# Kernel optimization log

Measured on AMD Instinct MI355X. Metric: run time of the kernel, lower is better.

## Reference

```python
import jax, jax.numpy as jnp
import numpy as np
import math

B = 32        # graphs in batch
N_PER = 2000  # nodes per graph
E_PER = 16000 # edges per graph
H = 256       # hidden_size
EF = 20       # edge_features
ET = 3        # edge_types
C = 100       # candidate nodes per graph
N = B * N_PER
E = B * E_PER


def setup_inputs() -> dict:
    key = jax.random.key(0)
    ks = jax.random.split(key, 12)
    embedding = jax.random.normal(ks[0], (N, H), dtype=jnp.float32)
    scores = jax.random.normal(ks[1], (N, 1), dtype=jnp.float32)
    offsets = jnp.arange(B, dtype=jnp.int64) * N_PER
    src = (jax.random.randint(ks[2], (B, E_PER), 0, N_PER) + offsets[:, None]).reshape(-1)
    dst = (jax.random.randint(ks[3], (B, E_PER), 0, N_PER) + offsets[:, None]).reshape(-1)
    etype = jax.random.randint(ks[4], (E,), 0, ET)
    cand_idx = offsets[:, None] + jnp.arange(C, dtype=jnp.int64)[None, :]  # [B, C]
    label = jax.random.randint(ks[5], (B,), 0, C)
    s = 1.0 / math.sqrt(H)
    Wl = jax.random.normal(ks[6], (H, H), dtype=jnp.float32) * s
    bl = jnp.zeros((H,), dtype=jnp.float32)
    Wr = jax.random.normal(ks[7], (H, H), dtype=jnp.float32) * s
    br = jnp.zeros((H,), dtype=jnp.float32)
    We = jax.random.normal(ks[8], (H, EF), dtype=jnp.float32) * (1.0 / math.sqrt(EF))
    be = jnp.zeros((H,), dtype=jnp.float32)
    edge_emb = jax.random.normal(ks[9], (ET, EF), dtype=jnp.float32)
    return {"embedding": embedding, "scores": scores, "Wl": Wl, "bl": bl,
            "Wr": Wr, "br": br, "We": We, "be": be, "edge_emb": edge_emb,
            "src": src, "dst": dst, "etype": etype, "cand_idx": cand_idx,
            "label": label}


def reference(embedding, scores, Wl, bl, Wr, br, We, be, edge_emb,
              src, dst, etype, cand_idx, label):
    # dropout is identity in eval mode
    h = embedding
    # edge type features: GELU(Embedding(type))  (torch GELU = exact erf form)
    ef = jax.nn.gelu(edge_emb[etype], approximate=False)          # [E, EF]
    attn_q = h @ Wl.T + bl                                         # [N, H]
    attn_k1 = h @ Wr.T + br                                        # [N, H]
    attn_k2 = ef @ We.T + be                                       # [E, H]
    # u_add_e: src node key + edge key
    attn_k = attn_k1[src] + attn_k2                                # [E, H]
    # v_dot_e: dst query dot edge key, scaled
    alpha = jnp.sum(attn_q[dst] * attn_k, axis=-1) / jnp.sqrt(jnp.float32(H))  # [E]
    # edge_softmax over incoming edges of each dst node
    seg_max = jax.ops.segment_max(alpha, dst, num_segments=N)
    ex = jnp.exp(alpha - seg_max[dst])
    seg_sum = jax.ops.segment_sum(ex, dst, num_segments=N)
    a = ex / seg_sum[dst]                                          # [E]
    # u_mul_e + sum aggregation: scatter-sum of src scores weighted by attention
    upd = jax.ops.segment_sum(scores[src] * a[:, None], dst, num_segments=N)  # [N, 1]
    # per-graph candidate logits and CE loss
    logits = upd[cand_idx.reshape(-1)].reshape(B, C)               # [B, C]
    logp = jax.nn.log_softmax(logits, axis=-1)
    loss = -jnp.sum(logp[jnp.arange(B), label])
    return loss, logits
```

## Files before the change

### kernel.cpp

```cpp
#include <hip/hip_runtime.h>
#include <hip/hip_bf16.h>
#include <float.h>
#include <math.h>

#define NB 32
#define NPER 2000
#define EPER 16000
#define HID 256
#define EFD 20
#define ETN 3
#define CN 100
#define NTOT (NB*NPER)
#define ETOT (NB*EPER)

#define QDELTA (6.0f/127.0f)
#define QINV   (127.0f/6.0f)

using f32x4  = __attribute__((ext_vector_type(4))) float;
using bf16x8 = __attribute__((ext_vector_type(8))) short;
using ushort8= __attribute__((ext_vector_type(8))) unsigned short;
using u32x4  = __attribute__((ext_vector_type(4))) unsigned int;

__device__ __forceinline__ unsigned short f2bf(float f){
  union{float f; unsigned int i;}v; v.f=f; unsigned int x=v.i;
  return (unsigned short)((x + 0x7fffu + ((x>>16)&1u)) >> 16);
}
__device__ __forceinline__ unsigned int cvt_pk_bf16(float lo, float hi){
  unsigned int r;
  asm("v_cvt_pk_bf16_f32 %0, %1, %2" : "=v"(r) : "v"(lo), "v"(hi));
  return r;
}
__device__ __forceinline__ void dot4i8(int& acc, unsigned int a, unsigned int b){
  asm("v_dot4_i32_i8 %0, %1, %2, %0" : "+v"(acc) : "v"(a), "v"(b));
}
__device__ __forceinline__ int sel4(int4 v, int i){
  int r = v.x;
  r = (i==1) ? v.y : r;
  r = (i==2) ? v.z : r;
  r = (i==3) ? v.w : r;
  return r;
}

__global__ __launch_bounds__(256) void setup_kernel(
    const float* __restrict__ Wl, const float* __restrict__ Wr,
    const float* __restrict__ We, const float* __restrict__ be,
    const float* __restrict__ edge_emb,
    unsigned short* __restrict__ Wlsw, unsigned short* __restrict__ Wrsw,
    signed char* __restrict__ k2q, float* __restrict__ k2scale,
    float* __restrict__ seg, float* __restrict__ out)
{
  __shared__ float k2f[ETN*HID];
  __shared__ float redmax[256];
  int b = blockIdx.x, t = threadIdx.x;
  if (b < 500) {
    int i = b*256 + t;
    seg[i] = 0.0f;
    if (i == 0) out[0] = 0.0f;
  } else if (b < 564) {
    int u = (b-500)*256 + t;
    int mat  = u >> 13;
    int v    = u & 8191;
    int cblk = v >> 9;
    int r    = v & 511;
    int kblk = r >> 6;
    int lane = r & 63;
    int col  = (cblk<<4) | (lane&15);
    int kk   = (kblk<<5) | ((lane>>4)<<3);
    const float* Wsrc = mat ? Wr : Wl;
    const f32x4* p = (const f32x4*)(Wsrc + col*HID + kk);
    f32x4 x0 = p[0], x1 = p[1];
    ushort8 w;
    w[0]=f2bf(x0[0]); w[1]=f2bf(x0[1]); w[2]=f2bf(x0[2]); w[3]=f2bf(x0[3]);
    w[4]=f2bf(x1[0]); w[5]=f2bf(x1[1]); w[6]=f2bf(x1[2]); w[7]=f2bf(x1[3]);
    *(ushort8*)((mat ? Wrsw : Wlsw) + (size_t)v*8) = w;
  } else {
    int j = t;
    float lmax = 0.0f;
    for (int ty=0; ty<ETN; ty++){
      float acc = be[j];
      for (int f=0; f<EFD; f++){
        float x = edge_emb[ty*EFD+f];
        float g = 0.5f*x*(1.0f + erff(x*0.7071067811865476f));
        acc += g * We[j*EFD+f];
      }
      k2f[ty*HID + j] = acc;
      lmax = fmaxf(lmax, fabsf(acc));
    }
    redmax[t] = lmax; __syncthreads();
    for (int sd=128; sd>0; sd>>=1){
      if (t < sd) redmax[t] = fmaxf(redmax[t], redmax[t+sd]);
      __syncthreads();
    }
    float d2 = fmaxf(redmax[0], 1e-20f) * (1.0f/127.0f);
    for (int ty=0; ty<ETN; ty++){
      int qv = (int)rintf(k2f[ty*HID+j] / d2);
      qv = min(127, max(-127, qv));
      k2q[ty*HID + j] = (signed char)qv;
    }
    if (t == 0) k2scale[0] = d2;
  }
}

#define BM 64
#define BK 64
#define LDA 72

__global__ __launch_bounds__(512) void gemm_qk(
    const float* __restrict__ h,
    const unsigned short* __restrict__ Wlsw, const unsigned short* __restrict__ Wrsw,
    const float* __restrict__ bl, const float* __restrict__ br,
    signed char* __restrict__ Qi8, signed char* __restrict__ K1i8)
{
  __shared__ unsigned short As[BM*LDA];

  int bm = blockIdx.x;
  int tid = threadIdx.x;
  int lane = tid & 63;
  int wv = tid >> 6;
  int wm = wv >> 2;
  int wn = wv & 3;

  f32x4 accQ[2][4], accK[2][4];
  #pragma unroll
  for(int i=0;i<2;i++)
    #pragma unroll
    for(int j=0;j<4;j++)
      #pragma unroll
      for(int r=0;r<4;r++){ accQ[i][j][r]=0.0f; accK[i][j][r]=0.0f; }

  const float* Arow = h + (size_t)bm*BM*HID;
  int arow = tid >> 3;
  int acs  = (tid & 7) * 8;

  f32x4 cur0 = *(const f32x4*)(Arow + arow*HID + acs);
  f32x4 cur1 = *(const f32x4*)(Arow + arow*HID + acs + 4);

  #pragma unroll
  for (int kt = 0; kt < 4; ++kt) {
    u32x4 aw;
    aw[0] = cvt_pk_bf16(cur0[0], cur0[1]);
    aw[1] = cvt_pk_bf16(cur0[2], cur0[3]);
    aw[2] = cvt_pk_bf16(cur1[0], cur1[1]);
    aw[3] = cvt_pk_bf16(cur1[2], cur1[3]);
    *(u32x4*)(&As[arow*LDA + acs]) = aw;
    __syncthreads();

    if (kt < 3) {
      cur0 = *(const f32x4*)(Arow + arow*HID + (kt+1)*BK + acs);
      cur1 = *(const f32x4*)(Arow + arow*HID + (kt+1)*BK + acs + 4);
    }

    #pragma unroll
    for (int ks = 0; ks < 2; ++ks) {
      int kblk = kt*2 + ks;
      int kb = ks*32 + (lane>>4)*8;
      bf16x8 af[2], lf[4], rf[4];
      #pragma unroll
      for (int fm=0; fm<2; fm++){
        int r0 = wm*32 + fm*16 + (lane&15);
        af[fm] = *(const bf16x8*)(&As[r0*LDA + kb]);
      }
      #pragma unroll
      for (int fn=0; fn<4; fn++){
        int cblk = wn*4 + fn;
        size_t o = ((size_t)(cblk*8 + kblk)*64 + lane)*8;
        lf[fn] = *(const bf16x8*)(Wlsw + o);
        rf[fn] = *(const bf16x8*)(Wrsw + o);
      }
      #pragma unroll
      for (int fm=0; fm<2; fm++)
        #pragma unroll
        for (int fn=0; fn<4; fn++){
          accQ[fm][fn] = __builtin_amdgcn_mfma_f32_16x16x32_bf16(af[fm], lf[fn], accQ[fm][fn], 0,0,0);
          accK[fm][fn] = __builtin_amdgcn_mfma_f32_16x16x32_bf16(af[fm], rf[fn], accK[fm][fn], 0,0,0);
        }
    }
    __syncthreads();
  }

  #pragma unroll
  for (int fn=0; fn<4; fn++){
    int col = wn*64 + fn*16 + (lane&15);
    float blv = bl[col], brv = br[col];
    #pragma unroll
    for (int fm=0; fm<2; fm++){
      int row0 = bm*BM + wm*32 + fm*16 + ((lane>>4)<<2);
      #pragma unroll
      for (int r=0; r<4; r++){
        size_t o = (size_t)(row0+r)*HID + col;
        int qv = (int)rintf((accQ[fm][fn][r] + blv) * QINV);
        int kv = (int)rintf((accK[fm][fn][r] + brv) * QINV);
        Qi8[o]  = (signed char)min(127, max(-127, qv));
        K1i8[o] = (signed char)min(127, max(-127, kv));
      }
    }
  }
}

__global__ __launch_bounds__(256) void tdot_kernel(
    const signed char* __restrict__ Qi8, const signed char* __restrict__ k2q,
    const float* __restrict__ k2scale, float* __restrict__ T)
{
  __shared__ unsigned int k2s[ETN*64];
  for (int i=threadIdx.x; i<ETN*64; i+=256)
    k2s[i] = ((const unsigned int*)k2q)[i];
  __syncthreads();

  int tid = threadIdx.x;
  int sl = tid & 15;
  int n = blockIdx.x*16 + (tid>>4);
  u32x4 q  = ((const u32x4*)(Qi8 + (size_t)n*HID))[sl];
  u32x4 c0 = ((const u32x4*)(k2s))[sl];
  u32x4 c1 = ((const u32x4*)(k2s + 64))[sl];
  u32x4 c2 = ((const u32x4*)(k2s + 128))[sl];
  int a0=0, a1=0, a2=0;
  #pragma unroll
  for (int w2=0; w2<4; w2++){
    dot4i8(a0, q[w2], c0[w2]);
    dot4i8(a1, q[w2], c1[w2]);
    dot4i8(a2, q[w2], c2[w2]);
  }
  #pragma unroll
  for (int m=1;m<16;m<<=1){
    a0 += __shfl_xor(a0, m);
    a1 += __shfl_xor(a1, m);
    a2 += __shfl_xor(a2, m);
  }
  if (sl==0){
    float sc = QDELTA * k2scale[0];
    f32x4 tv; tv[0]=a0*sc; tv[1]=a1*sc; tv[2]=a2*sc; tv[3]=0.f;
    *(f32x4*)(T + (size_t)n*4) = tv;
  }
}

__global__ __launch_bounds__(256) void edge_attn(
    const signed char* __restrict__ Qi8, const signed char* __restrict__ K1i8,
    const float* __restrict__ T,
    const int* __restrict__ src, const int* __restrict__ dst, const int* __restrict__ ety,
    const float* __restrict__ scores,
    float* __restrict__ seg)
{
  int bid = blockIdx.x;
  int xcd = bid & 7;
  int slot = bid >> 3;
  int grp = slot / 250;
  int within = slot - grp*250;
  int graph = grp*8 + xcd;

  int tid = threadIdx.x;
  int sl = tid & 15;
  int g = tid >> 4;
  int e0 = graph*EPER + within*64 + g*4;

  int4 sv4 = *(const int4*)(src + e0);
  int4 dv4 = *(const int4*)(dst + e0);
  int4 tv4 = *(const int4*)(ety + e0);

  u32x4 q0 = ((const u32x4*)(Qi8  + (size_t)dv4.x*HID))[sl];
  u32x4 k0 = ((const u32x4*)(K1i8 + (size_t)sv4.x*HID))[sl];
  u32x4 q1 = ((const u32x4*)(Qi8  + (size_t)dv4.y*HID))[sl];
  u32x4 k1 = ((const u32x4*)(K1i8 + (size_t)sv4.y*HID))[sl];
  u32x4 q2 = ((const u32x4*)(Qi8  + (size_t)dv4.z*HID))[sl];
  u32x4 k2 = ((const u32x4*)(K1i8 + (size_t)sv4.z*HID))[sl];
  u32x4 q3 = ((const u32x4*)(Qi8  + (size_t)dv4.w*HID))[sl];
  u32x4 k3 = ((const u32x4*)(K1i8 + (size_t)sv4.w*HID))[sl];

  int a0=0, a1=0, a2=0, a3=0;
  #pragma unroll
  for (int w2=0; w2<4; w2++){
    dot4i8(a0, q0[w2], k0[w2]);
    dot4i8(a1, q1[w2], k1[w2]);
    dot4i8(a2, q2[w2], k2[w2]);
    dot4i8(a3, q3[w2], k3[w2]);
  }
  #pragma unroll
  for (int m=1;m<16;m<<=1){
    a0 += __shfl_xor(a0, m);
    a1 += __shfl_xor(a1, m);
    a2 += __shfl_xor(a2, m);
    a3 += __shfl_xor(a3, m);
  }
  if (sl < 8){
    int j = sl & 3;
    int role = sl >> 2;
    int dn = sel4(dv4, j);
    int sn = sel4(sv4, j);
    int tn = sel4(tv4, j);
    float av = (float)a0;
    av = (j==1) ? (float)a1 : av;
    av = (j==2) ? (float)a2 : av;
    av = (j==3) ? (float)a3 : av;
    const float DD = QDELTA*QDELTA;
    float ex = expf((av*DD + T[(size_t)dn*4 + tn]) * 0.0625f);
    float val = role ? ex * scores[sn] : ex;
    atomicAdd(&seg[2*dn + role], val);
  }
}

__global__ __launch_bounds__(128) void logits_kernel(
    const float* __restrict__ seg,
    const int* __restrict__ cand, const int* __restrict__ label,
    float* __restrict__ out)
{
  __shared__ float red[128];
  __shared__ float lvals[CN];
  int b = blockIdx.x;
  int t = threadIdx.x;
  float v = -FLT_MAX;
  if (t < CN){
    int node = cand[b*CN + t];
    float ss = seg[2*node];
    float u = (ss > 0.0f) ? (seg[2*node+1]/ss) : 0.0f;
    lvals[t] = u;
    out[1 + b*CN + t] = u;
    v = u;
  }
  red[t] = v; __syncthreads();
  for (int sd=64; sd>0; sd>>=1){
    if (t < sd) red[t] = fmaxf(red[t], red[t+sd]);
    __syncthreads();
  }
  float mx = red[0];
  __syncthreads();
  float sv = (t < CN) ? expf(lvals[t]-mx) : 0.0f;
  red[t] = sv; __syncthreads();
  for (int sd=64; sd>0; sd>>=1){
    if (t < sd) red[t] += red[t+sd];
    __syncthreads();
  }
  if (t==0){
    float lse = mx + logf(red[0]);
    atomicAdd(out, -(lvals[label[b]] - lse));
  }
}

extern "C" void kernel_launch(void* const* d_in, const int* in_sizes, int n_in,
                              void* d_out, int out_size, void* d_ws, size_t ws_size,
                              hipStream_t stream) {
  const float* emb      = (const float*)d_in[0];
  const float* scores   = (const float*)d_in[1];
  const float* Wl       = (const float*)d_in[2];
  const float* blb      = (const float*)d_in[3];
  const float* Wr       = (const float*)d_in[4];
  const float* brb      = (const float*)d_in[5];
  const float* We       = (const float*)d_in[6];
  const float* be       = (const float*)d_in[7];
  const float* edge_emb = (const float*)d_in[8];
  const int* src   = (const int*)d_in[9];
  const int* dst   = (const int*)d_in[10];
  const int* ety   = (const int*)d_in[11];
  const int* cand  = (const int*)d_in[12];
  const int* label = (const int*)d_in[13];
  float* out = (float*)d_out;

  char* w = (char*)d_ws;
  size_t off = 0;
  auto alloc = [&](size_t bytes)->char* {
    char* p = w + off; off += (bytes + 255) & ~(size_t)255; return p;
  };
  signed char*    Qi8  = (signed char*)alloc((size_t)NTOT*HID);
  signed char*    K1i8 = (signed char*)alloc((size_t)NTOT*HID);
  unsigned short* Wlsw = (unsigned short*)alloc((size_t)HID*HID*2);
  unsigned short* Wrsw = (unsigned short*)alloc((size_t)HID*HID*2);
  signed char*    k2q  = (signed char*)alloc((size_t)ETN*HID);
  float* k2scale = (float*)alloc(4);
  float* T      = (float*)alloc((size_t)NTOT*4*4);
  float* seg    = (float*)alloc((size_t)NTOT*8);
  (void)ws_size; (void)in_sizes; (void)n_in; (void)out_size;

  setup_kernel<<<dim3(565), dim3(256), 0, stream>>>(Wl, Wr, We, be, edge_emb,
                                                    Wlsw, Wrsw, k2q, k2scale, seg, out);
  gemm_qk<<<dim3(NTOT/BM), dim3(512), 0, stream>>>(emb, Wlsw, Wrsw, blb, brb, Qi8, K1i8);
  tdot_kernel<<<dim3(NTOT/16), dim3(256), 0, stream>>>(Qi8, k2q, k2scale, T);
  edge_attn<<<dim3(ETOT/64), dim3(256), 0, stream>>>(Qi8, K1i8, T, src, dst, ety, scores,
                                                     seg);
  logits_kernel<<<dim3(NB), dim3(128), 0, stream>>>(seg, cand, label, out);
}
```

Baseline: 199.2 us.

## Drop LDS staging in QK GEMM and process eight edges per group in attention

The projection GEMM no longer stages the bf16-converted activation tile in shared memory. Each wave loads its fp32 rows directly into MFMA fragments, and each block covers 256 rows by 64 columns, so the grid becomes 1000 blocks. This removes LDS writes and barriers, but each activation row is now re-read from global memory by four column-slice blocks. The edge attention kernel now handles 8 edges per 16-lane group instead of 4, halving the grid and using all 16 lanes for the atomic stage, at the cost of more registers and more gather loads in flight per thread.

```diff
diff --git a/kernel.cpp b/kernel.cpp
--- a/kernel.cpp
+++ b/kernel.cpp
@@ -39,6 +39,11 @@
   r = (i==2) ? v.z : r;
   r = (i==3) ? v.w : r;
   return r;
+}
+__device__ __forceinline__ int sel8(int4 a, int4 b, int i){
+  int lo = sel4(a, i&3);
+  int hi = sel4(b, i&3);
+  return (i&4) ? hi : lo;
 }
 
 __global__ __launch_bounds__(256) void setup_kernel(
@@ -101,24 +106,22 @@
   }
 }
 
-#define BM 64
-#define BK 64
-#define LDA 72
-
 __global__ __launch_bounds__(512) void gemm_qk(
     const float* __restrict__ h,
     const unsigned short* __restrict__ Wlsw, const unsigned short* __restrict__ Wrsw,
     const float* __restrict__ bl, const float* __restrict__ br,
     signed char* __restrict__ Qi8, signed char* __restrict__ K1i8)
 {
-  __shared__ unsigned short As[BM*LDA];
-
-  int bm = blockIdx.x;
+  int bid = blockIdx.x;
+  int rc = bid >> 2;
+  int cs = bid & 3;
   int tid = threadIdx.x;
   int lane = tid & 63;
   int wv = tid >> 6;
-  int wm = wv >> 2;
-  int wn = wv & 3;
+
+  int rowf = rc*256 + wv*32 + (lane&15);
+  int kb_lane = (lane>>4)*8;
+  int C0 = cs*64;
 
   f32x4 accQ[2][4], accK[2][4];
   #pragma unroll
@@ -128,63 +131,44 @@
       #pragma unroll
       for(int r=0;r<4;r++){ accQ[i][j][r]=0.0f; accK[i][j][r]=0.0f; }
 
-  const float* Arow = h + (size_t)bm*BM*HID;
-  int arow = tid >> 3;
-  int acs  = (tid & 7) * 8;
-
-  f32x4 cur0 = *(const f32x4*)(Arow + arow*HID + acs);
-  f32x4 cur1 = *(const f32x4*)(Arow + arow*HID + acs + 4);
-
-  #pragma unroll
-  for (int kt = 0; kt < 4; ++kt) {
-    u32x4 aw;
-    aw[0] = cvt_pk_bf16(cur0[0], cur0[1]);
-    aw[1] = cvt_pk_bf16(cur0[2], cur0[3]);
-    aw[2] = cvt_pk_bf16(cur1[0], cur1[1]);
-    aw[3] = cvt_pk_bf16(cur1[2], cur1[3]);
-    *(u32x4*)(&As[arow*LDA + acs]) = aw;
-    __syncthreads();
-
-    if (kt < 3) {
-      cur0 = *(const f32x4*)(Arow + arow*HID + (kt+1)*BK + acs);
-      cur1 = *(const f32x4*)(Arow + arow*HID + (kt+1)*BK + acs + 4);
-    }
-
-    #pragma unroll
-    for (int ks = 0; ks < 2; ++ks) {
-      int kblk = kt*2 + ks;
-      int kb = ks*32 + (lane>>4)*8;
-      bf16x8 af[2], lf[4], rf[4];
-      #pragma unroll
-      for (int fm=0; fm<2; fm++){
-        int r0 = wm*32 + fm*16 + (lane&15);
-        af[fm] = *(const bf16x8*)(&As[r0*LDA + kb]);
-      }
+  #pragma unroll
+  for (int kblk = 0; kblk < 8; ++kblk) {
+    int k0 = kblk*32 + kb_lane;
+    bf16x8 af[2], lf[4], rf[4];
+    #pragma unroll
+    for (int fm=0; fm<2; fm++){
+      const float* p = h + (size_t)(rowf + fm*16)*HID + k0;
+      f32x4 x0 = *(const f32x4*)p;
+      f32x4 x1 = *(const f32x4*)(p + 4);
+      u32x4 aw;
+      aw[0] = cvt_pk_bf16(x0[0], x0[1]);
+      aw[1] = cvt_pk_bf16(x0[2], x0[3]);
+      aw[2] = cvt_pk_bf16(x1[0], x1[1]);
+      aw[3] = cvt_pk_bf16(x1[2], x1[3]);
+      af[fm] = *(bf16x8*)&aw;
+    }
+    #pragma unroll
+    for (int fn=0; fn<4; fn++){
+      size_t o = ((size_t)((cs*4 + fn)*8 + kblk)*64 + lane)*8;
+      lf[fn] = *(const bf16x8*)(Wlsw + o);
+      rf[fn] = *(const bf16x8*)(Wrsw + o);
+    }
+    #pragma unroll
+    for (int fm=0; fm<2; fm++)
       #pragma unroll
       for (int fn=0; fn<4; fn++){
-        int cblk = wn*4 + fn;
-        size_t o = ((size_t)(cblk*8 + kblk)*64 + lane)*8;
-        lf[fn] = *(const bf16x8*)(Wlsw + o);
-        rf[fn] = *(const bf16x8*)(Wrsw + o);
+        accQ[fm][fn] = __builtin_amdgcn_mfma_f32_16x16x32_bf16(af[fm], lf[fn], accQ[fm][fn], 0,0,0);
+        accK[fm][fn] = __builtin_amdgcn_mfma_f32_16x16x32_bf16(af[fm], rf[fn], accK[fm][fn], 0,0,0);
       }
-      #pragma unroll
-      for (int fm=0; fm<2; fm++)
-        #pragma unroll
-        for (int fn=0; fn<4; fn++){
-          accQ[fm][fn] = __builtin_amdgcn_mfma_f32_16x16x32_bf16(af[fm], lf[fn], accQ[fm][fn], 0,0,0);
-          accK[fm][fn] = __builtin_amdgcn_mfma_f32_16x16x32_bf16(af[fm], rf[fn], accK[fm][fn], 0,0,0);
-        }
-    }
-    __syncthreads();
   }
 
   #pragma unroll
   for (int fn=0; fn<4; fn++){
-    int col = wn*64 + fn*16 + (lane&15);
+    int col = C0 + fn*16 + (lane&15);
     float blv = bl[col], brv = br[col];
     #pragma unroll
     for (int fm=0; fm<2; fm++){
-      int row0 = bm*BM + wm*32 + fm*16 + ((lane>>4)<<2);
+      int row0 = rc*256 + wv*32 + fm*16 + ((lane>>4)<<2);
       #pragma unroll
       for (int r=0; r<4; r++){
         size_t o = (size_t)(row0+r)*HID + col;
@@ -243,53 +227,59 @@
   int bid = blockIdx.x;
   int xcd = bid & 7;
   int slot = bid >> 3;
-  int grp = slot / 250;
-  int within = slot - grp*250;
+  int grp = slot / 125;
+  int within = slot - grp*125;
   int graph = grp*8 + xcd;
 
   int tid = threadIdx.x;
   int sl = tid & 15;
   int g = tid >> 4;
-  int e0 = graph*EPER + within*64 + g*4;
-
-  int4 sv4 = *(const int4*)(src + e0);
-  int4 dv4 = *(const int4*)(dst + e0);
-  int4 tv4 = *(const int4*)(ety + e0);
-
-  u32x4 q0 = ((const u32x4*)(Qi8  + (size_t)dv4.x*HID))[sl];
-  u32x4 k0 = ((const u32x4*)(K1i8 + (size_t)sv4.x*HID))[sl];
-  u32x4 q1 = ((const u32x4*)(Qi8  + (size_t)dv4.y*HID))[sl];
-  u32x4 k1 = ((const u32x4*)(K1i8 + (size_t)sv4.y*HID))[sl];
-  u32x4 q2 = ((const u32x4*)(Qi8  + (size_t)dv4.z*HID))[sl];
-  u32x4 k2 = ((const u32x4*)(K1i8 + (size_t)sv4.z*HID))[sl];
-  u32x4 q3 = ((const u32x4*)(Qi8  + (size_t)dv4.w*HID))[sl];
-  u32x4 k3 = ((const u32x4*)(K1i8 + (size_t)sv4.w*HID))[sl];
-
-  int a0=0, a1=0, a2=0, a3=0;
-  #pragma unroll
-  for (int w2=0; w2<4; w2++){
-    dot4i8(a0, q0[w2], k0[w2]);
-    dot4i8(a1, q1[w2], k1[w2]);
-    dot4i8(a2, q2[w2], k2[w2]);
-    dot4i8(a3, q3[w2], k3[w2]);
-  }
-  #pragma unroll
-  for (int m=1;m<16;m<<=1){
-    a0 += __shfl_xor(a0, m);
-    a1 += __shfl_xor(a1, m);
-    a2 += __shfl_xor(a2, m);
-    a3 += __shfl_xor(a3, m);
-  }
-  if (sl < 8){
-    int j = sl & 3;
-    int role = sl >> 2;
-    int dn = sel4(dv4, j);
-    int sn = sel4(sv4, j);
-    int tn = sel4(tv4, j);
-    float av = (float)a0;
-    av = (j==1) ? (float)a1 : av;
-    av = (j==2) ? (float)a2 : av;
-    av = (j==3) ? (float)a3 : av;
+  int e0 = graph*EPER + within*128 + g*8;
+
+  int4 sa = *(const int4*)(src + e0);
+  int4 sb = *(const int4*)(src + e0 + 4);
+  int4 da = *(const int4*)(dst + e0);
+  int4 db = *(const int4*)(dst + e0 + 4);
+  int4 ta = *(const int4*)(ety + e0);
+  int4 tb = *(const int4*)(ety + e0 + 4);
+
+  u32x4 qv[8], kv[8];
+  #pragma unroll
+  for (int j=0; j<8; j++){
+    int dn = sel8(da, db, j);
+    int sn = sel8(sa, sb, j);
+    qv[j] = ((const u32x4*)(Qi8  + (size_t)dn*HID))[sl];
+    kv[j] = ((const u32x4*)(K1i8 + (size_t)sn*HID))[sl];
+  }
+
+  int ac[8];
+  #pragma unroll
+  for (int j=0; j<8; j++) ac[j] = 0;
+  #pragma unroll
+  for (int j=0; j<8; j++)
+    #pragma unroll
+    for (int w2=0; w2<4; w2++)
+      dot4i8(ac[j], qv[j][w2], kv[j][w2]);
+  #pragma unroll
+  for (int j=0; j<8; j++)
+    #pragma unroll
+    for (int m=1; m<16; m<<=1)
+      ac[j] += __shfl_xor(ac[j], m);
+
+  {
+    int j = sl & 7;
+    int role = sl >> 3;
+    int dn = sel8(da, db, j);
+    int sn = sel8(sa, sb, j);
+    int tn = sel8(ta, tb, j);
+    float av = (float)ac[0];
+    av = (j==1) ? (float)ac[1] : av;
+    av = (j==2) ? (float)ac[2] : av;
+    av = (j==3) ? (float)ac[3] : av;
+    av = (j==4) ? (float)ac[4] : av;
+    av = (j==5) ? (float)ac[5] : av;
+    av = (j==6) ? (float)ac[6] : av;
+    av = (j==7) ? (float)ac[7] : av;
     const float DD = QDELTA*QDELTA;
     float ex = expf((av*DD + T[(size_t)dn*4 + tn]) * 0.0625f);
     float val = role ? ex * scores[sn] : ex;
@@ -370,9 +360,9 @@
 
   setup_kernel<<<dim3(565), dim3(256), 0, stream>>>(Wl, Wr, We, be, edge_emb,
                                                     Wlsw, Wrsw, k2q, k2scale, seg, out);
-  gemm_qk<<<dim3(NTOT/BM), dim3(512), 0, stream>>>(emb, Wlsw, Wrsw, blb, brb, Qi8, K1i8);
+  gemm_qk<<<dim3(1000), dim3(512), 0, stream>>>(emb, Wlsw, Wrsw, blb, brb, Qi8, K1i8);
   tdot_kernel<<<dim3(NTOT/16), dim3(256), 0, stream>>>(Qi8, k2q, k2scale, T);
-  edge_attn<<<dim3(ETOT/64), dim3(256), 0, stream>>>(Qi8, K1i8, T, src, dst, ety, scores,
-                                                     seg);
+  edge_attn<<<dim3(ETOT/128), dim3(256), 0, stream>>>(Qi8, K1i8, T, src, dst, ety, scores,
+                                                      seg);
   logits_kernel<<<dim3(NB), dim3(128), 0, stream>>>(seg, cand, label, out);
 }
```

New measurement: 222.5 us. +11.7%, slower.
